# Kernel tuning notes

Measured on AMD Instinct MI355X. Metric: run time of the kernel, lower is better.

The kernel has to match this reference:

```python
import jax, jax.numpy as jnp
import numpy as np

B, TQ, TY = 8, 400, 400
Q_DIM, Y_DIM, ATT_DIM = 256, 256, 128


def setup_inputs() -> dict:
    key = jax.random.key(0)
    ks = jax.random.split(key, 9)
    s_q = 1.0 / np.sqrt(Q_DIM)
    s_y = 1.0 / np.sqrt(Y_DIM)
    s_a = 1.0 / np.sqrt(ATT_DIM)
    return {
        "query": jax.random.normal(ks[0], (B, TQ, Q_DIM), jnp.float32),
        "y": jax.random.normal(ks[1], (B, TY, Y_DIM), jnp.float32),
        "Wq_w": jax.random.uniform(ks[2], (ATT_DIM, Q_DIM), jnp.float32, -s_q, s_q),
        "Wq_b": jax.random.uniform(ks[3], (ATT_DIM,), jnp.float32, -s_q, s_q),
        "Wy_w": jax.random.uniform(ks[4], (ATT_DIM, Y_DIM), jnp.float32, -s_y, s_y),
        "Wy_b": jax.random.uniform(ks[5], (ATT_DIM,), jnp.float32, -s_y, s_y),
        "v_w": jax.random.uniform(ks[6], (1, ATT_DIM), jnp.float32, -s_a, s_a),
        "v_b": jax.random.uniform(ks[7], (1,), jnp.float32, -s_a, s_a),
        "n_wins_y": jax.random.randint(ks[8], (B,), TY // 2, TY + 1, jnp.int64 if jax.config.jax_enable_x64 else jnp.int32),
    }


def reference(query, y, Wq_w, Wq_b, Wy_w, Wy_b, v_w, v_b, n_wins_y):
    # Bahdanau scores: tanh(Wq(q)[:,None,:,:] + Wy(y)[:,:,None,:]) -> [B,Ty,Tq,A]
    q_proj = jnp.einsum('bqd,ad->bqa', query, Wq_w) + Wq_b      # [B,Tq,A]
    y_proj = jnp.einsum('btd,ad->bta', y, Wy_w) + Wy_b          # [B,Ty,A]
    h = jnp.tanh(q_proj[:, None, :, :] + y_proj[:, :, None, :])  # [B,Ty,Tq,A]
    att = jnp.einsum('btqa,a->btq', h, v_w[0]) + v_b[0]          # [B,Ty,Tq]
    att = jnp.transpose(att, (0, 2, 1))                          # [B,Tq,Ty]
    # mask invalid y windows (dim 2 = Ty), then softmax over Ty
    mask = jnp.arange(att.shape[2])[None, None, :] < n_wins_y[:, None, None]
    att = jnp.where(mask, att, -jnp.inf)
    att = jax.nn.softmax(att, axis=2)
    # soft attention apply: bmm(att, y) -> [B,Tq,y_dim]
    return jnp.einsum('bqt,btd->bqd', att, y)
```

## Files before the change

### kernel.cpp

```cpp
#include <hip/hip_runtime.h>


#define LOG2E 1.4426950408889634f
#define TANH_SCALE 2.8853900817779268f

constexpr int TQn = 400, TYn = 400, AD = 128, DD = 256;
constexpr int SSTR = 65;

__global__ __launch_bounds__(128) void transpose_kernel(
    const float* __restrict__ Wq, const float* __restrict__ Wy,
    float4* __restrict__ WTq, float4* __restrict__ WTy)
{
    const int k4 = blockIdx.x & 63;
    const bool isq = blockIdx.x < 64;
    const float4* src = reinterpret_cast<const float4*>(isq ? Wq : Wy);
    float4* dst = isq ? WTq : WTy;
    const int a = threadIdx.x;
    dst[k4 * 128 + a] = src[a * 64 + k4];
}

__global__ __launch_bounds__(256, 4) void proj_kernel(
    const float* __restrict__ qin, const float* __restrict__ yin,
    const float4* __restrict__ WTq, const float* __restrict__ bq,
    const float4* __restrict__ WTy, const float* __restrict__ by,
    float* __restrict__ Eq, float* __restrict__ Ey)
{
    const int blk = blockIdx.x;
    const bool is_q = blk < 400;
    const int row0 = (is_q ? blk : blk - 400) * 8;
    const float* in   = (is_q ? qin : yin) + (size_t)row0 * DD;
    const float4* wt  = is_q ? WTq : WTy;
    const float* bias = is_q ? bq : by;
    float* outp = (is_q ? Eq : Ey) + (size_t)row0 * AD;

    __shared__ float lin[8 * DD];
    __shared__ float red[8][AD];
    {
        const float4* in4 = reinterpret_cast<const float4*>(in);
        float4* l4s = reinterpret_cast<float4*>(lin);
        l4s[threadIdx.x]       = in4[threadIdx.x];
        l4s[threadIdx.x + 256] = in4[threadIdx.x + 256];
    }
    __syncthreads();

    const int a = threadIdx.x & 127;
    const int h = threadIdx.x >> 7;
    float acc[8] = {0.f,0.f,0.f,0.f,0.f,0.f,0.f,0.f};
    const float4* l4 = reinterpret_cast<const float4*>(lin);
    #pragma unroll 8
    for (int i = 0; i < 32; ++i) {
        const int k4 = h * 32 + i;
        float4 w4 = wt[k4 * 128 + a];
        #pragma unroll
        for (int r = 0; r < 8; ++r) {
            float4 v = l4[r * 64 + k4];
            acc[r] = fmaf(w4.x, v.x, acc[r]);
            acc[r] = fmaf(w4.y, v.y, acc[r]);
            acc[r] = fmaf(w4.z, v.z, acc[r]);
            acc[r] = fmaf(w4.w, v.w, acc[r]);
        }
    }
    if (h) {
        #pragma unroll
        for (int r = 0; r < 8; ++r) red[r][a] = acc[r];
    }
    __syncthreads();
    if (!h) {
        const float bb = bias[a];
        #pragma unroll
        for (int r = 0; r < 8; ++r)
            outp[(size_t)r * AD + a] =
                __builtin_amdgcn_exp2f((acc[r] + red[r][a] + bb) * TANH_SCALE);
    }
}

__global__ __launch_bounds__(256, 4) void score_kernel(
    const float* __restrict__ Eq,
    const float* __restrict__ Ey,
    const float* __restrict__ vw,
    const int*  __restrict__ nwins,
    float* __restrict__ s)
{
    const int bid = blockIdx.x;
    const int b   = bid / 700;
    const int rem = bid % 700;
    const int qg  = rem / 7;
    const int tt  = rem % 7;
    const int n   = nwins[b];
    const int t0  = tt * 64;
    if (t0 >= n) return;
    const int q0 = qg * 4;

    __shared__ float4 s_ey[32 * SSTR];
    __shared__ float4 s_eq4[4 * 32];
    __shared__ float4 s_v4[32];

    const int tid  = threadIdx.x;
    const int pcol = tid & 31;
    const int prow = tid >> 5;
    {
        const float4* eyb = reinterpret_cast<const float4*>(Ey);
        const size_t base = (size_t)(b * TYn) * 32 + pcol;
        #pragma unroll
        for (int k = 0; k < 8; ++k) {
            const int rt = min(t0 + prow + 8 * k, TYn - 1);
            s_ey[pcol * SSTR + prow + 8 * k] = eyb[base + (size_t)rt * 32];
        }
    }
    if (tid < 128) {
        s_eq4[tid] = reinterpret_cast<const float4*>(Eq + (size_t)(b * TQn + q0) * AD)[tid];
    } else if (tid < 160) {
        float4 v = reinterpret_cast<const float4*>(vw)[tid - 128];
        s_v4[tid - 128] = make_float4(-2.f * v.x, -2.f * v.y, -2.f * v.z, -2.f * v.w);
    }
    __syncthreads();

    const int lane = tid & 63;
    const int wave = tid >> 6;
    const int tloc = (wave << 4) | (lane & 15);
    const int ag   = lane >> 4;
    float ac0 = 0.f, ac1 = 0.f, ac2 = 0.f, ac3 = 0.f;
    #pragma unroll
    for (int i = 0; i < 8; ++i) {
        const int a4 = ag * 8 + i;
        const float4 yv = s_ey[a4 * SSTR + tloc];
        const float4 vv = s_v4[a4];
        #define SCORE_Q(ACC, QQ)                                            \
        {                                                                   \
            float4 qv = s_eq4[(QQ) * 32 + a4];                              \
            float a0 = fmaf(qv.x, yv.x, 1.f);                               \
            float a1 = fmaf(qv.y, yv.y, 1.f);                               \
            float a2 = fmaf(qv.z, yv.z, 1.f);                               \
            float a3 = fmaf(qv.w, yv.w, 1.f);                               \
            float p01 = a0 * a1, p23 = a2 * a3;                             \
            float R = __builtin_amdgcn_rcpf(p01 * p23);                     \
            float u = p23 * R, w = p01 * R;                                 \
            ACC = fmaf(vv.x, a1 * u, ACC);                                  \
            ACC = fmaf(vv.y, a0 * u, ACC);                                  \
            ACC = fmaf(vv.z, a3 * w, ACC);                                  \
            ACC = fmaf(vv.w, a2 * w, ACC);                                  \
        }
        SCORE_Q(ac0, 0) SCORE_Q(ac1, 1) SCORE_Q(ac2, 2) SCORE_Q(ac3, 3)
        #undef SCORE_Q
    }
    ac0 += __shfl_xor(ac0, 16, 64); ac0 += __shfl_xor(ac0, 32, 64);
    ac1 += __shfl_xor(ac1, 16, 64); ac1 += __shfl_xor(ac1, 32, 64);
    ac2 += __shfl_xor(ac2, 16, 64); ac2 += __shfl_xor(ac2, 32, 64);
    ac3 += __shfl_xor(ac3, 16, 64); ac3 += __shfl_xor(ac3, 32, 64);
    const int t = t0 + tloc;
    if (ag == 0 && t < TYn) {
        const size_t o = (size_t)(b * TQn + q0) * TYn + t;
        s[o]            = ac0;
        s[o + TYn]      = ac1;
        s[o + 2 * TYn]  = ac2;
        s[o + 3 * TYn]  = ac3;
    }
}

__global__ __launch_bounds__(256, 4) void apply_kernel(
    const float* __restrict__ y,
    const float* __restrict__ s,
    const int*  __restrict__ nwins,
    float* __restrict__ out)
{
    const int bid = blockIdx.x;
    const int b   = bid / 100;
    const int q0  = (bid % 100) * 4;
    const int tid = threadIdx.x, wave = tid >> 6, lane = tid & 63;
    const int n = nwins[b];
    const float NEG_INF = -__builtin_inff();

    __shared__ float  s_p[4][408];
    __shared__ float4 s_y[2][16 * 64];

    const float4* yb = reinterpret_cast<const float4*>(y) + (size_t)(b * TYn) * 64;
    const int scol = tid & 63, srow0 = tid >> 6;
    float4 g0 = yb[(size_t)(srow0     ) * 64 + scol];
    float4 g1 = yb[(size_t)(srow0 +  4) * 64 + scol];
    float4 g2 = yb[(size_t)(srow0 +  8) * 64 + scol];
    float4 g3 = yb[(size_t)(srow0 + 12) * 64 + scol];

    const float* srow = s + (size_t)(b * TQn + q0 + wave) * TYn;
    float sc0, sc1, sc2, sc3, sc4, sc5, sc6;
    {
        int t;
        t = 0 * 64 + lane; sc0 = (t < n) ? srow[t] : NEG_INF;
        t = 1 * 64 + lane; sc1 = (t < n) ? srow[t] : NEG_INF;
        t = 2 * 64 + lane; sc2 = (t < n) ? srow[t] : NEG_INF;
        t = 3 * 64 + lane; sc3 = (t < n) ? srow[t] : NEG_INF;
        t = 4 * 64 + lane; sc4 = (t < n) ? srow[t] : NEG_INF;
        t = 5 * 64 + lane; sc5 = (t < n) ? srow[t] : NEG_INF;
        t = 6 * 64 + lane; sc6 = (t < n) ? srow[t] : NEG_INF;
    }
    float m = fmaxf(fmaxf(fmaxf(sc0, sc1), fmaxf(sc2, sc3)),
                    fmaxf(fmaxf(sc4, sc5), sc6));
    #pragma unroll
    for (int off = 32; off >= 1; off >>= 1) m = fmaxf(m, __shfl_xor(m, off, 64));
    sc0 = __builtin_amdgcn_exp2f((sc0 - m) * LOG2E);
    sc1 = __builtin_amdgcn_exp2f((sc1 - m) * LOG2E);
    sc2 = __builtin_amdgcn_exp2f((sc2 - m) * LOG2E);
    sc3 = __builtin_amdgcn_exp2f((sc3 - m) * LOG2E);
    sc4 = __builtin_amdgcn_exp2f((sc4 - m) * LOG2E);
    sc5 = __builtin_amdgcn_exp2f((sc5 - m) * LOG2E);
    sc6 = __builtin_amdgcn_exp2f((sc6 - m) * LOG2E);
    float l = ((sc0 + sc1) + (sc2 + sc3)) + ((sc4 + sc5) + sc6);
    #pragma unroll
    for (int off = 32; off >= 1; off >>= 1) l += __shfl_xor(l, off, 64);
    const float inv = 1.0f / l;
    s_p[wave][0 * 64 + lane] = sc0 * inv;
    s_p[wave][1 * 64 + lane] = sc1 * inv;
    s_p[wave][2 * 64 + lane] = sc2 * inv;
    s_p[wave][3 * 64 + lane] = sc3 * inv;
    s_p[wave][4 * 64 + lane] = sc4 * inv;
    s_p[wave][5 * 64 + lane] = sc5 * inv;
    {
        const int t = 6 * 64 + lane;
        if (t < TYn) s_p[wave][t] = sc6 * inv;
    }

    const int q  = lane >> 4;
    const int d4 = (wave << 4) | (lane & 15);
    float4 acc = {0.f, 0.f, 0.f, 0.f};
    const int ntile = (n + 15) >> 4;

    __syncthreads();
    for (int i = 0; i < ntile; ++i) {
        float4* buf = s_y[i & 1];
        buf[(srow0     ) * 64 + scol] = g0;
        buf[(srow0 +  4) * 64 + scol] = g1;
        buf[(srow0 +  8) * 64 + scol] = g2;
        buf[(srow0 + 12) * 64 + scol] = g3;
        if (i + 1 < ntile) {
            const int t0n = (i + 1) * 16;
            g0 = yb[(size_t)(t0n + srow0     ) * 64 + scol];
            g1 = yb[(size_t)(t0n + srow0 +  4) * 64 + scol];
            g2 = yb[(size_t)(t0n + srow0 +  8) * 64 + scol];
            g3 = yb[(size_t)(t0n + srow0 + 12) * 64 + scol];
        }
        __syncthreads();
        const int tb = i * 16;
        #pragma unroll
        for (int ttl = 0; ttl < 16; ++ttl) {
            const float  pt = s_p[q][tb + ttl];
            const float4 yv = buf[ttl * 64 + d4];
            acc.x = fmaf(pt, yv.x, acc.x);
            acc.y = fmaf(pt, yv.y, acc.y);
            acc.z = fmaf(pt, yv.z, acc.z);
            acc.w = fmaf(pt, yv.w, acc.w);
        }
    }
    reinterpret_cast<float4*>(out)[(size_t)(b * TQn + q0 + q) * 64 + d4] = acc;
}

extern "C" void kernel_launch(void* const* d_in, const int* in_sizes, int n_in,
                              void* d_out, int out_size, void* d_ws, size_t ws_size,
                              hipStream_t stream) {
    const float* query = (const float*)d_in[0];
    const float* y     = (const float*)d_in[1];
    const float* Wq_w  = (const float*)d_in[2];
    const float* Wq_b  = (const float*)d_in[3];
    const float* Wy_w  = (const float*)d_in[4];
    const float* Wy_b  = (const float*)d_in[5];
    const float* v_w   = (const float*)d_in[6];
    const int* nw      = (const int*)d_in[8];
    float* out = (float*)d_out;

    float4* WTq = (float4*)d_ws;
    float4* WTy = WTq + 64 * 128;
    float*  Eq  = (float*)(WTy + 64 * 128);
    float*  Ey  = Eq + (size_t)8 * TQn * AD;
    float*  s   = Ey + (size_t)8 * TYn * AD;

    transpose_kernel<<<128, 128, 0, stream>>>(Wq_w, Wy_w, WTq, WTy);
    proj_kernel<<<800, 256, 0, stream>>>(query, y, WTq, Wq_b, WTy, Wy_b, Eq, Ey);
    score_kernel<<<8 * 100 * 7, 256, 0, stream>>>(Eq, Ey, v_w, nw, s);
    apply_kernel<<<8 * 100, 256, 0, stream>>>(y, s, nw, out);
}
```

Before: 65.87 us.

## Drop shared-memory staging across proj, score and apply kernels; transpose Ey layout

The projection kernel now uses 128 threads that each compute a full dot product, reading inputs directly from global memory with no shared-memory reduction. It writes Ey in an a4-major transposed layout so the score kernel can load it coalesced without LDS staging. The score kernel now handles one t per lane across all 128 attention dimensions, which removes the shuffle reduction. The -2*v prescale moves into the transpose kernel. The apply kernel processes 8 queries per block, reads y directly from global/L2, and drops the double-buffered LDS tiles. This trades LDS traffic and barriers for more global and cache reads plus lower occupancy per block.

New measurement: 106.2 us. 1.61x slower.

```diff
diff --git a/kernel.cpp b/kernel.cpp
--- a/kernel.cpp
+++ b/kernel.cpp
@@ -5,11 +5,14 @@
 #define TANH_SCALE 2.8853900817779268f
 
 constexpr int TQn = 400, TYn = 400, AD = 128, DD = 256;
-constexpr int SSTR = 65;
+constexpr int EYLD = 8 * TYn;
+constexpr int PROW = 404;
 
 __global__ __launch_bounds__(128) void transpose_kernel(
     const float* __restrict__ Wq, const float* __restrict__ Wy,
-    float4* __restrict__ WTq, float4* __restrict__ WTy)
+    const float* __restrict__ vw,
+    float4* __restrict__ WTq, float4* __restrict__ WTy,
+    float* __restrict__ vneg)
 {
     const int k4 = blockIdx.x & 63;
     const bool isq = blockIdx.x < 64;
@@ -17,168 +20,124 @@
     float4* dst = isq ? WTq : WTy;
     const int a = threadIdx.x;
     dst[k4 * 128 + a] = src[a * 64 + k4];
-}
-
-__global__ __launch_bounds__(256, 4) void proj_kernel(
+    if (blockIdx.x == 0) vneg[a] = -2.f * vw[a];
+}
+
+__global__ __launch_bounds__(128) void proj_kernel(
     const float* __restrict__ qin, const float* __restrict__ yin,
     const float4* __restrict__ WTq, const float* __restrict__ bq,
     const float4* __restrict__ WTy, const float* __restrict__ by,
-    float* __restrict__ Eq, float* __restrict__ Ey)
+    float* __restrict__ Eq, float* __restrict__ EyT)
 {
     const int blk = blockIdx.x;
     const bool is_q = blk < 400;
     const int row0 = (is_q ? blk : blk - 400) * 8;
-    const float* in   = (is_q ? qin : yin) + (size_t)row0 * DD;
+    const float4* in4 = reinterpret_cast<const float4*>(
+        (is_q ? qin : yin) + (size_t)row0 * DD);
     const float4* wt  = is_q ? WTq : WTy;
     const float* bias = is_q ? bq : by;
-    float* outp = (is_q ? Eq : Ey) + (size_t)row0 * AD;
-
-    __shared__ float lin[8 * DD];
-    __shared__ float red[8][AD];
-    {
-        const float4* in4 = reinterpret_cast<const float4*>(in);
-        float4* l4s = reinterpret_cast<float4*>(lin);
-        l4s[threadIdx.x]       = in4[threadIdx.x];
-        l4s[threadIdx.x + 256] = in4[threadIdx.x + 256];
-    }
-    __syncthreads();
-
-    const int a = threadIdx.x & 127;
-    const int h = threadIdx.x >> 7;
+
+    const int a = threadIdx.x;
     float acc[8] = {0.f,0.f,0.f,0.f,0.f,0.f,0.f,0.f};
-    const float4* l4 = reinterpret_cast<const float4*>(lin);
-    #pragma unroll 8
-    for (int i = 0; i < 32; ++i) {
-        const int k4 = h * 32 + i;
-        float4 w4 = wt[k4 * 128 + a];
+    for (int c = 0; c < 8; ++c) {
+        float4 wreg[8];
+        #pragma unroll
+        for (int j = 0; j < 8; ++j)
+            wreg[j] = wt[(c * 8 + j) * 128 + a];
         #pragma unroll
         for (int r = 0; r < 8; ++r) {
-            float4 v = l4[r * 64 + k4];
-            acc[r] = fmaf(w4.x, v.x, acc[r]);
-            acc[r] = fmaf(w4.y, v.y, acc[r]);
-            acc[r] = fmaf(w4.z, v.z, acc[r]);
-            acc[r] = fmaf(w4.w, v.w, acc[r]);
+            #pragma unroll
+            for (int j = 0; j < 8; ++j) {
+                float4 v = in4[r * 64 + c * 8 + j];
+                acc[r] = fmaf(wreg[j].x, v.x, acc[r]);
+                acc[r] = fmaf(wreg[j].y, v.y, acc[r]);
+                acc[r] = fmaf(wreg[j].z, v.z, acc[r]);
+                acc[r] = fmaf(wreg[j].w, v.w, acc[r]);
+            }
         }
     }
-    if (h) {
-        #pragma unroll
-        for (int r = 0; r < 8; ++r) red[r][a] = acc[r];
-    }
-    __syncthreads();
-    if (!h) {
-        const float bb = bias[a];
-        #pragma unroll
-        for (int r = 0; r < 8; ++r)
-            outp[(size_t)r * AD + a] =
-                __builtin_amdgcn_exp2f((acc[r] + red[r][a] + bb) * TANH_SCALE);
-    }
-}
-
-__global__ __launch_bounds__(256, 4) void score_kernel(
+    const float bb = bias[a];
+    #pragma unroll
+    for (int r = 0; r < 8; ++r) {
+        const float e = __builtin_amdgcn_exp2f((acc[r] + bb) * TANH_SCALE);
+        if (is_q) Eq[(size_t)(row0 + r) * AD + a] = e;
+        else      EyT[(size_t)(a >> 2) * (EYLD * 4) + (size_t)(row0 + r) * 4 + (a & 3)] = e;
+    }
+}
+
+__global__ __launch_bounds__(128) void score_kernel(
     const float* __restrict__ Eq,
-    const float* __restrict__ Ey,
-    const float* __restrict__ vw,
+    const float4* __restrict__ EyT4,
+    const float* __restrict__ vneg,
     const int*  __restrict__ nwins,
     float* __restrict__ s)
 {
-    const int bid = blockIdx.x;
-    const int b   = bid / 700;
-    const int rem = bid % 700;
-    const int qg  = rem / 7;
-    const int tt  = rem % 7;
-    const int n   = nwins[b];
-    const int t0  = tt * 64;
-    if (t0 >= n) return;
+    const int bid  = blockIdx.x;
+    const int b    = bid / 400;
+    const int rem  = bid % 400;
+    const int qg   = rem / 4;
+    const int pair = rem % 4;
+    const int n = nwins[b];
+    const int ntile = (n + 63) >> 6;
+    if (pair * 2 >= ntile) return;
+    const int tile = pair * 2 + (threadIdx.x >> 6);
+    const int lane = threadIdx.x & 63;
     const int q0 = qg * 4;
 
-    __shared__ float4 s_ey[32 * SSTR];
-    __shared__ float4 s_eq4[4 * 32];
-    __shared__ float4 s_v4[32];
-
-    const int tid  = threadIdx.x;
-    const int pcol = tid & 31;
-    const int prow = tid >> 5;
-    {
-        const float4* eyb = reinterpret_cast<const float4*>(Ey);
-        const size_t base = (size_t)(b * TYn) * 32 + pcol;
-        #pragma unroll
-        for (int k = 0; k < 8; ++k) {
-            const int rt = min(t0 + prow + 8 * k, TYn - 1);
-            s_ey[pcol * SSTR + prow + 8 * k] = eyb[base + (size_t)rt * 32];
+    const float4* eq4 = reinterpret_cast<const float4*>(Eq)
+                      + (size_t)(b * TQn + q0) * 32;
+    const float4* vn4 = reinterpret_cast<const float4*>(vneg);
+
+    if (tile < ntile) {
+        const int t = tile * 64 + lane;
+        const int col = b * TYn + min(t, TYn - 1);
+        float ac0 = 0.f, ac1 = 0.f, ac2 = 0.f, ac3 = 0.f;
+        #pragma unroll 8
+        for (int a4 = 0; a4 < 32; ++a4) {
+            const float4 ey = EyT4[(size_t)a4 * EYLD + col];
+            const float4 vv = vn4[a4];
+            #define SCORE_Q(ACC, QQ)                                        \
+            {                                                               \
+                const float4 qv = eq4[(QQ) * 32 + a4];  \
+                float a0 = fmaf(qv.x, ey.x, 1.f);                           \
+                float a1 = fmaf(qv.y, ey.y, 1.f);                           \
+                float a2 = fmaf(qv.z, ey.z, 1.f);                           \
+                float a3 = fmaf(qv.w, ey.w, 1.f);                           \
+                float p01 = a0 * a1, p23 = a2 * a3;                         \
+                float R = __builtin_amdgcn_rcpf(p01 * p23);                 \
+                float u = p23 * R, w = p01 * R;                             \
+                ACC = fmaf(vv.x, a1 * u, ACC);                              \
+                ACC = fmaf(vv.y, a0 * u, ACC);                              \
+                ACC = fmaf(vv.z, a3 * w, ACC);                              \
+                ACC = fmaf(vv.w, a2 * w, ACC);                              \
+            }
+            SCORE_Q(ac0, 0) SCORE_Q(ac1, 1) SCORE_Q(ac2, 2) SCORE_Q(ac3, 3)
+            #undef SCORE_Q
         }
-    }
-    if (tid < 128) {
-        s_eq4[tid] = reinterpret_cast<const float4*>(Eq + (size_t)(b * TQn + q0) * AD)[tid];
-    } else if (tid < 160) {
-        float4 v = reinterpret_cast<const float4*>(vw)[tid - 128];
-        s_v4[tid - 128] = make_float4(-2.f * v.x, -2.f * v.y, -2.f * v.z, -2.f * v.w);
-    }
-    __syncthreads();
-
-    const int lane = tid & 63;
-    const int wave = tid >> 6;
-    const int tloc = (wave << 4) | (lane & 15);
-    const int ag   = lane >> 4;
-    float ac0 = 0.f, ac1 = 0.f, ac2 = 0.f, ac3 = 0.f;
-    #pragma unroll
-    for (int i = 0; i < 8; ++i) {
-        const int a4 = ag * 8 + i;
-        const float4 yv = s_ey[a4 * SSTR + tloc];
-        const float4 vv = s_v4[a4];
-        #define SCORE_Q(ACC, QQ)                                            \
-        {                                                                   \
-            float4 qv = s_eq4[(QQ) * 32 + a4];                              \
-            float a0 = fmaf(qv.x, yv.x, 1.f);                               \
-            float a1 = fmaf(qv.y, yv.y, 1.f);                               \
-            float a2 = fmaf(qv.z, yv.z, 1.f);                               \
-            float a3 = fmaf(qv.w, yv.w, 1.f);                               \
-            float p01 = a0 * a1, p23 = a2 * a3;                             \
-            float R = __builtin_amdgcn_rcpf(p01 * p23);                     \
-            float u = p23 * R, w = p01 * R;                                 \
-            ACC = fmaf(vv.x, a1 * u, ACC);                                  \
-            ACC = fmaf(vv.y, a0 * u, ACC);                                  \
-            ACC = fmaf(vv.z, a3 * w, ACC);                                  \
-            ACC = fmaf(vv.w, a2 * w, ACC);                                  \
+        if (t < TYn) {
+            float* srow = s + (size_t)(b * TQn + q0) * TYn + t;
+            srow[0]           = ac0;
+            srow[TYn]         = ac1;
+            srow[2 * TYn]     = ac2;
+            srow[3 * TYn]     = ac3;
         }
-        SCORE_Q(ac0, 0) SCORE_Q(ac1, 1) SCORE_Q(ac2, 2) SCORE_Q(ac3, 3)
-        #undef SCORE_Q
-    }
-    ac0 += __shfl_xor(ac0, 16, 64); ac0 += __shfl_xor(ac0, 32, 64);
-    ac1 += __shfl_xor(ac1, 16, 64); ac1 += __shfl_xor(ac1, 32, 64);
-    ac2 += __shfl_xor(ac2, 16, 64); ac2 += __shfl_xor(ac2, 32, 64);
-    ac3 += __shfl_xor(ac3, 16, 64); ac3 += __shfl_xor(ac3, 32, 64);
-    const int t = t0 + tloc;
-    if (ag == 0 && t < TYn) {
-        const size_t o = (size_t)(b * TQn + q0) * TYn + t;
-        s[o]            = ac0;
-        s[o + TYn]      = ac1;
-        s[o + 2 * TYn]  = ac2;
-        s[o + 3 * TYn]  = ac3;
-    }
-}
-
-__global__ __launch_bounds__(256, 4) void apply_kernel(
+    }
+}
+
+__global__ __launch_bounds__(512, 2) void apply_kernel(
     const float* __restrict__ y,
     const float* __restrict__ s,
     const int*  __restrict__ nwins,
     float* __restrict__ out)
 {
     const int bid = blockIdx.x;
-    const int b   = bid / 100;
-    const int q0  = (bid % 100) * 4;
+    const int b   = bid / 50;
+    const int q0  = (bid % 50) * 8;
     const int tid = threadIdx.x, wave = tid >> 6, lane = tid & 63;
     const int n = nwins[b];
     const float NEG_INF = -__builtin_inff();
 
-    __shared__ float  s_p[4][408];
-    __shared__ float4 s_y[2][16 * 64];
-
-    const float4* yb = reinterpret_cast<const float4*>(y) + (size_t)(b * TYn) * 64;
-    const int scol = tid & 63, srow0 = tid >> 6;
-    float4 g0 = yb[(size_t)(srow0     ) * 64 + scol];
-    float4 g1 = yb[(size_t)(srow0 +  4) * 64 + scol];
-    float4 g2 = yb[(size_t)(srow0 +  8) * 64 + scol];
-    float4 g3 = yb[(size_t)(srow0 + 12) * 64 + scol];
+    __shared__ __align__(16) float s_p[8][PROW];
 
     const float* srow = s + (size_t)(b * TQn + q0 + wave) * TYn;
     float sc0, sc1, sc2, sc3, sc4, sc5, sc6;
@@ -217,37 +176,29 @@
         const int t = 6 * 64 + lane;
         if (t < TYn) s_p[wave][t] = sc6 * inv;
     }
-
-    const int q  = lane >> 4;
-    const int d4 = (wave << 4) | (lane & 15);
+    __syncthreads();
+
+    const int q  = lane >> 3;
+    const int d4 = (wave << 3) | (lane & 7);
+    const float4* prow4 = reinterpret_cast<const float4*>(&s_p[q][0]);
+    const float4* yb4 = reinterpret_cast<const float4*>(y) + (size_t)(b * TYn) * 64;
     float4 acc = {0.f, 0.f, 0.f, 0.f};
-    const int ntile = (n + 15) >> 4;
-
-    __syncthreads();
-    for (int i = 0; i < ntile; ++i) {
-        float4* buf = s_y[i & 1];
-        buf[(srow0     ) * 64 + scol] = g0;
-        buf[(srow0 +  4) * 64 + scol] = g1;
-        buf[(srow0 +  8) * 64 + scol] = g2;
-        buf[(srow0 + 12) * 64 + scol] = g3;
-        if (i + 1 < ntile) {
-            const int t0n = (i + 1) * 16;
-            g0 = yb[(size_t)(t0n + srow0     ) * 64 + scol];
-            g1 = yb[(size_t)(t0n + srow0 +  4) * 64 + scol];
-            g2 = yb[(size_t)(t0n + srow0 +  8) * 64 + scol];
-            g3 = yb[(size_t)(t0n + srow0 + 12) * 64 + scol];
-        }
-        __syncthreads();
-        const int tb = i * 16;
-        #pragma unroll
-        for (int ttl = 0; ttl < 16; ++ttl) {
-            const float  pt = s_p[q][tb + ttl];
-            const float4 yv = buf[ttl * 64 + d4];
-            acc.x = fmaf(pt, yv.x, acc.x);
-            acc.y = fmaf(pt, yv.y, acc.y);
-            acc.z = fmaf(pt, yv.z, acc.z);
-            acc.w = fmaf(pt, yv.w, acc.w);
-        }
+    const int n4q = (n + 3) >> 2;
+    for (int tq = 0; tq < n4q; ++tq) {
+        const float4 pv = prow4[tq];
+        const float4* yr = yb4 + (size_t)(tq * 4) * 64;
+        const float4 y0 = yr[d4];
+        const float4 y1 = yr[64 + d4];
+        const float4 y2 = yr[128 + d4];
+        const float4 y3 = yr[192 + d4];
+        acc.x = fmaf(pv.x, y0.x, acc.x); acc.y = fmaf(pv.x, y0.y, acc.y);
+        acc.z = fmaf(pv.x, y0.z, acc.z); acc.w = fmaf(pv.x, y0.w, acc.w);
+        acc.x = fmaf(pv.y, y1.x, acc.x); acc.y = fmaf(pv.y, y1.y, acc.y);
+        acc.z = fmaf(pv.y, y1.z, acc.z); acc.w = fmaf(pv.y, y1.w, acc.w);
+        acc.x = fmaf(pv.z, y2.x, acc.x); acc.y = fmaf(pv.z, y2.y, acc.y);
+        acc.z = fmaf(pv.z, y2.z, acc.z); acc.w = fmaf(pv.z, y2.w, acc.w);
+        acc.x = fmaf(pv.w, y3.x, acc.x); acc.y = fmaf(pv.w, y3.y, acc.y);
+        acc.z = fmaf(pv.w, y3.z, acc.z); acc.w = fmaf(pv.w, y3.w, acc.w);
     }
     reinterpret_cast<float4*>(out)[(size_t)(b * TQn + q0 + q) * 64 + d4] = acc;
 }
@@ -265,14 +216,16 @@
     const int* nw      = (const int*)d_in[8];
     float* out = (float*)d_out;
 
-    float4* WTq = (float4*)d_ws;
-    float4* WTy = WTq + 64 * 128;
-    float*  Eq  = (float*)(WTy + 64 * 128);
-    float*  Ey  = Eq + (size_t)8 * TQn * AD;
-    float*  s   = Ey + (size_t)8 * TYn * AD;
-
-    transpose_kernel<<<128, 128, 0, stream>>>(Wq_w, Wy_w, WTq, WTy);
-    proj_kernel<<<800, 256, 0, stream>>>(query, y, WTq, Wq_b, WTy, Wy_b, Eq, Ey);
-    score_kernel<<<8 * 100 * 7, 256, 0, stream>>>(Eq, Ey, v_w, nw, s);
-    apply_kernel<<<8 * 100, 256, 0, stream>>>(y, s, nw, out);
-}
+    float4* WTq  = (float4*)d_ws;
+    float4* WTy  = WTq + 64 * 128;
+    float*  vneg = (float*)(WTy + 64 * 128);
+    float*  Eq   = vneg + 1024;
+    float*  EyT  = Eq + (size_t)8 * TQn * AD;
+    float*  s    = EyT + (size_t)32 * EYLD * 4;
+
+    transpose_kernel<<<128, 128, 0, stream>>>(Wq_w, Wy_w, v_w, WTq, WTy, vneg);
+    proj_kernel<<<800, 128, 0, stream>>>(query, y, WTq, Wq_b, WTy, Wy_b, Eq, EyT);
+    score_kernel<<<8 * 100 * 4, 128, 0, stream>>>(
+        Eq, (const float4*)EyT, vneg, nw, s);
+    apply_kernel<<<8 * 50, 512, 0, stream>>>(y, s, nw, out);
+}
```
